# Kernel tuning notes

Hardware: AMD Instinct MI355X
Metric: run time of the kernel (lower is better)

Reference implementation:

```python
import jax, jax.numpy as jnp
import numpy as np

B, S, H = 8, 4096, 2048
E, F, K = 32, 128, 2
UTIL_BONUS = 0.1
CAP_PENALTY = 0.1


def setup_inputs() -> dict:
    key = jax.random.key(0)
    ks = jax.random.split(key, 4)
    hidden = jax.random.normal(ks[0], (B, S, H), dtype=jnp.float32)
    router_w = 0.02 * jax.random.normal(ks[1], (E, H), dtype=jnp.float32)
    router_b = jnp.zeros((E,), dtype=jnp.float32)
    w1 = 0.02 * jax.random.normal(ks[2], (E, F, H), dtype=jnp.float32)
    b1 = jnp.zeros((E, F), dtype=jnp.float32)
    w2 = 0.02 * jax.random.normal(ks[3], (E, H, F), dtype=jnp.float32)
    b2 = jnp.zeros((E, H), dtype=jnp.float32)
    activation_counts = jnp.zeros((E,), dtype=jnp.float32)
    expert_drift = jnp.zeros((E,), dtype=jnp.float32)
    return {"hidden": hidden, "router_w": router_w, "router_b": router_b,
            "w1": w1, "b1": b1, "w2": w2, "b2": b2,
            "activation_counts": activation_counts, "expert_drift": expert_drift}


def reference(hidden, router_w, router_b, w1, b1, w2, b2, activation_counts, expert_drift):
    # --- router with usage bonus / capacity penalty (buffers are zero at init) ---
    pooled = hidden.mean(axis=1)                      # [B, H]
    base_logits = pooled @ router_w.T + router_b      # [B, E]
    total = activation_counts.sum()
    usage = activation_counts / jnp.maximum(total, 1e-8)
    bonus = jnp.where(total > 0.0, UTIL_BONUS * (1.0 - usage), jnp.zeros_like(usage))
    usage_norm = activation_counts / jnp.maximum(activation_counts.max(), 1e-8)
    drift_norm = expert_drift / jnp.maximum(expert_drift.max(), 1e-8)
    penalty = CAP_PENALTY * 0.5 * (usage_norm + drift_norm)
    logits = base_logits + bonus[None, :] - penalty[None, :]
    router_probs = jax.nn.softmax(logits, axis=-1)    # [B, E]

    topk_probs, topk_idx = jax.lax.top_k(router_probs, K)  # [B, K]
    topk_probs = topk_probs / jnp.maximum(topk_probs.sum(axis=-1, keepdims=True), 1e-8)

    # --- gather selected expert weights and apply to the full sequence ---
    W1 = w1[topk_idx]   # [B, K, F, H]
    B1 = b1[topk_idx]   # [B, K, F]
    W2 = w2[topk_idx]   # [B, K, H, F]
    B2 = b2[topk_idx]   # [B, K, H]

    h1 = jnp.einsum('bsh,bkfh->bksf', hidden, W1) + B1[:, :, None, :]
    h1 = jax.nn.gelu(h1, approximate=False)           # torch nn.GELU default = exact erf
    out = jnp.einsum('bksf,bkhf->bksh', h1, W2) + B2[:, :, None, :]
    delta = jnp.einsum('bk,bksh->bsh', topk_probs, out)  # weighted combine
    return delta, topk_idx, topk_probs, router_probs
```

## Files before the change

kernel.cpp:

```cpp
#include <hip/hip_runtime.h>
#include <hip/hip_bf16.h>

#define BB 8
#define SS 4096
#define HH 2048
#define EE 32
#define FF 128

constexpr size_t DELTA_N = (size_t)BB * SS * HH;
constexpr size_t WELEM = (size_t)EE * FF * HH;
constexpr size_t WBYTES = WELEM * 2;

typedef short bf16x8 __attribute__((ext_vector_type(8)));
typedef float f32x4 __attribute__((ext_vector_type(4)));
typedef unsigned short u16;
typedef __attribute__((address_space(3))) unsigned char as3u8;
typedef __attribute__((address_space(1))) const unsigned char as1u8;

__device__ __forceinline__ u16 f2bfu(float x) {
  unsigned int u = __float_as_uint(x);
  u = (u + 0x7FFFu + ((u >> 16) & 1u)) >> 16;
  return (u16)u;
}

__device__ __forceinline__ unsigned int pk2(float a, float b) {
  union { __hip_bfloat162 h; unsigned int u; } c;
  c.h = __float22bfloat162_rn(make_float2(a, b));
  return c.u;
}

__device__ __forceinline__ bf16x8 pack8(float4 a, float4 b) {
  union { bf16x8 v; unsigned int u[4]; } r;
  r.u[0] = pk2(a.x, a.y);
  r.u[1] = pk2(a.z, a.w);
  r.u[2] = pk2(b.x, b.y);
  r.u[3] = pk2(b.z, b.w);
  return r.v;
}

__device__ __forceinline__ uint4 cvt4(float4 a, float4 b) {
  return make_uint4(pk2(a.x, a.y), pk2(a.z, a.w), pk2(b.x, b.y), pk2(b.z, b.w));
}

__device__ __forceinline__ void glds16(const void* g, void* l) {
  __builtin_amdgcn_global_load_lds((as1u8*)g, (as3u8*)l, 16, 0, 0);
}

__global__ void k_zero(float* __restrict__ ws) {
  if (threadIdx.x < 288) ws[threadIdx.x] = 0.0f;
}

__global__ void k_pool_logits(const float* __restrict__ hidden,
                              const float* __restrict__ rw,
                              float* __restrict__ logits) {
  const int b  = blockIdx.x >> 6;
  const int hc = (blockIdx.x >> 3) & 7;
  const int sq = blockIdx.x & 7;
  const int t  = threadIdx.x;
  const int tx = t & 63;
  const int qq = t >> 6;
  const int h0 = hc * 256;

  const float* p = hidden + ((size_t)b * SS + sq * 512 + qq * 128) * HH + h0 + tx * 4;
  float4 s = make_float4(0.f, 0.f, 0.f, 0.f);
  for (int i = 0; i < 128; ++i) {
    float4 v = *(const float4*)(p + (size_t)i * HH);
    s.x += v.x; s.y += v.y; s.z += v.z; s.w += v.w;
  }
  __shared__ float ps[4][256];
  __shared__ float pl[256];
  *(float4*)&ps[qq][tx * 4] = s;
  __syncthreads();
  pl[t] = ps[0][t] + ps[1][t] + ps[2][t] + ps[3][t];
  __syncthreads();

  const int e = t >> 3, part = t & 7;
  const float* wrp = rw + (size_t)e * HH + h0 + part * 32;
  float v = 0.f;
#pragma unroll
  for (int m = 0; m < 32; ++m) v += pl[part * 32 + m] * wrp[m];
  v += __shfl_xor(v, 1, 8);
  v += __shfl_xor(v, 2, 8);
  v += __shfl_xor(v, 4, 8);
  if (part == 0) atomicAdd(&logits[b * EE + e], v * (1.0f / (float)SS));
}

__global__ void k_topk(const float* __restrict__ logits, const float* __restrict__ rb,
                       const float* __restrict__ counts, const float* __restrict__ drift,
                       int* __restrict__ sel, float* __restrict__ pscale,
                       float* __restrict__ out) {
  int t = threadIdx.x;
  int b = t >> 5, e = t & 31;
  float total = 0.0f, cmax = 0.0f, dmax = 0.0f;
  for (int i = 0; i < EE; ++i) {
    float c = counts[i]; total += c; cmax = fmaxf(cmax, c);
    float d = drift[i];  dmax = fmaxf(dmax, d);
  }
  float cnt = counts[e], dr = drift[e];
  float usage = cnt / fmaxf(total, 1e-8f);
  float bonus = (total > 0.0f) ? 0.1f * (1.0f - usage) : 0.0f;
  float un = cnt / fmaxf(cmax, 1e-8f);
  float dn = dr / fmaxf(dmax, 1e-8f);
  float l = logits[t] + rb[e] + bonus - 0.05f * (un + dn);

  float m = l;
  for (int w = 16; w; w >>= 1) m = fmaxf(m, __shfl_xor(m, w, 32));
  float p = expf(l - m);
  float ssum = p;
  for (int w = 16; w; w >>= 1) ssum += __shfl_xor(ssum, w, 32);
  float prob = p / ssum;
  out[DELTA_N + 32 + t] = prob;

  float v1 = prob; int i1 = e;
  for (int w = 16; w; w >>= 1) {
    float ov = __shfl_xor(v1, w, 32); int oi = __shfl_xor(i1, w, 32);
    if (ov > v1 || (ov == v1 && oi < i1)) { v1 = ov; i1 = oi; }
  }
  float v2 = (e == i1) ? -1.0f : prob; int i2 = e;
  for (int w = 16; w; w >>= 1) {
    float ov = __shfl_xor(v2, w, 32); int oi = __shfl_xor(i2, w, 32);
    if (ov > v2 || (ov == v2 && oi < i2)) { v2 = ov; i2 = oi; }
  }
  if (e == 0) {
    float denom = fmaxf(v1 + v2, 1e-8f);
    float tp0 = v1 / denom, tp1 = v2 / denom;
    sel[b * 2 + 0] = i1;
    sel[b * 2 + 1] = i2;
    pscale[b * 2 + 0] = tp0;
    pscale[b * 2 + 1] = tp1;
    out[DELTA_N + 0 + b * 2 + 0] = (float)i1;
    out[DELTA_N + 0 + b * 2 + 1] = (float)i2;
    out[DELTA_N + 16 + b * 2 + 0] = tp0;
    out[DELTA_N + 16 + b * 2 + 1] = tp1;
  }
}

__global__ void k_pack(const float* __restrict__ w1, const float* __restrict__ w2,
                       u16* __restrict__ w1p, u16* __restrict__ w2p) {
  unsigned c = blockIdx.x * 256 + threadIdx.x;
  const float* src;
  u16* dst;
  if (c < 1048576u) {
    unsigned e = c >> 15, ci = c & 32767u;
    unsigned it = ci >> 10;
    unsigned cb = (ci & 1023u) * 16u;
    unsigned col = cb >> 7;
    unsigned kb = (cb & 127u) ^ ((col & 7u) << 4);
    unsigned k = it * 64u + (kb >> 1);
    src = w1 + ((size_t)(e * 128u + col) * HH + k);
    dst = w1p + (size_t)c * 8;
  } else {
    unsigned c2 = c - 1048576u;
    unsigned e = c2 >> 15, ci = c2 & 32767u;
    unsigned h = ci >> 4;
    unsigned cb = (ci & 15u) * 16u;
    unsigned kb = cb ^ ((h & 7u) << 4);
    unsigned f = kb >> 1;
    src = w2 + ((size_t)(e * 2048u + h) * FF + f);
    dst = w2p + (size_t)c2 * 8;
  }
  float4 a = *(const float4*)src;
  float4 b = *(const float4*)(src + 4);
  *(bf16x8*)dst = pack8(a, b);
}

#define SB_OFF 32768
#define T_OFF 65536

__global__ __launch_bounds__(512, 2) void k_ffn2(
    const float* __restrict__ hidden, const float* __restrict__ bs1,
    const float* __restrict__ bs2, const u16* __restrict__ w1p,
    const u16* __restrict__ w2p, const int* __restrict__ sel,
    const float* __restrict__ pscale, float* __restrict__ out) {
  __shared__ __align__(16) char smem[131072];

  const int t    = threadIdx.x;
  const int lane = t & 63;
  const int wv   = t >> 6;
  const int wr   = wv >> 2;
  const int wc   = wv & 3;
  const int l15  = lane & 15;
  const int lk   = lane >> 4;

  const int bid = blockIdx.x;
  const int b   = bid & 7;
  const int s0  = (bid >> 3) * 128;

  const int e0 = sel[2 * b], e1 = sel[2 * b + 1];
  const float p0 = pscale[2 * b], p1 = pscale[2 * b + 1];

  const int RB  = wr * 64;
  const int CBc = wc * 64;
  const int CB2 = wc * 32;

  const char* w1pb = (const char*)w1p;
  const char* w2pb = (const char*)w2p;

  const int arow = t >> 2;
  const int akq2 = (t & 3) * 32;
  const float* hA = hidden + ((size_t)b * SS + s0 + arow) * HH + (t & 3) * 16;
  const unsigned swA = (arow & 7) << 4;

  const size_t esel = (size_t)(wv < 4 ? e0 : e1);
  const char* w1src = w1pb + esel * 524288 + (size_t)(wv & 3) * 4096 + (size_t)lane * 16;
  char* sbW = &smem[SB_OFF + wv * 4096];

  f32x4 zero = {0.f, 0.f, 0.f, 0.f};
  f32x4 acc1[4][4];
#pragma unroll
  for (int i = 0; i < 4; ++i)
#pragma unroll
    for (int j = 0; j < 4; ++j) acc1[i][j] = zero;

  {
    float4 P[4];
#pragma unroll
    for (int q = 0; q < 4; ++q) P[q] = *(const float4*)(hA + q * 4);
#pragma unroll
    for (int r = 0; r < 4; ++r) glds16(w1src + r * 1024, sbW + r * 1024);
    char* da = &smem[arow * 128];
    *(uint4*)(da + (akq2 ^ swA)) = cvt4(P[0], P[1]);
    *(uint4*)(da + ((akq2 + 16) ^ swA)) = cvt4(P[2], P[3]);
  }
  __syncthreads();

  for (int j = 0; j < 32; ++j) {
    const int cb = j & 1, nb = cb ^ 1;
    float4 P[4];
    if (j < 31) {
      const float* hp = hA + (j + 1) * 64;
#pragma unroll
      for (int q = 0; q < 4; ++q) P[q] = *(const float4*)(hp + q * 4);
      const char* s = w1src + (size_t)(j + 1) * 16384;
      char* d = sbW + nb * 32768;
#pragma unroll
      for (int r = 0; r < 4; ++r) glds16(s + r * 1024, d + r * 1024);
    }
    const char* sa = &smem[cb * 16384];
    const char* sb = &smem[SB_OFF + cb * 32768];
#pragma unroll
    for (int kk = 0; kk < 2; ++kk) {
      bf16x8 af[4], bfv[4];
#pragma unroll
      for (int rt = 0; rt < 4; ++rt) {
        int row = RB + rt * 16 + l15;
        af[rt] = *(const bf16x8*)(sa + row * 128 + ((kk * 64 + lk * 16) ^ ((row & 7) << 4)));
      }
#pragma unroll
      for (int ct = 0; ct < 4; ++ct) {
        int col = CBc + ct * 16 + l15;
        bfv[ct] = *(const bf16x8*)(sb + col * 128 + ((kk * 64 + lk * 16) ^ ((col & 7) << 4)));
      }
#pragma unroll
      for (int rt = 0; rt < 4; ++rt)
#pragma unroll
        for (int ct = 0; ct < 4; ++ct)
          acc1[rt][ct] = __builtin_amdgcn_mfma_f32_16x16x32_bf16(af[rt], bfv[ct], acc1[rt][ct], 0, 0, 0);
    }
    if (j < 31) {
      char* da = &smem[nb * 16384 + arow * 128];
      *(uint4*)(da + (akq2 ^ swA)) = cvt4(P[0], P[1]);
      *(uint4*)(da + ((akq2 + 16) ^ swA)) = cvt4(P[2], P[3]);
    }
    __syncthreads();
  }

#pragma unroll
  for (int ct = 0; ct < 4; ++ct) {
    int c = CBc + ct * 16 + l15;
    int ec = (c < 128) ? e0 : e1;
    float pc = (c < 128) ? p0 : p1;
    float bias = bs1[ec * FF + (c & 127)];
#pragma unroll
    for (int rt = 0; rt < 4; ++rt)
#pragma unroll
      for (int r = 0; r < 4; ++r) {
        int row = RB + rt * 16 + lk * 4 + r;
        float x = acc1[rt][ct][r] + bias;
        float g = 0.5f * x * (1.0f + erff(x * 0.70710678118654752f));
        *(u16*)&smem[row * 512 + ((c * 2) ^ ((row & 7) << 4))] = f2bfu(pc * g);
      }
  }
  {
    const char* s = w2pb + (size_t)e0 * 524288 + (size_t)wv * 4096 + (size_t)lane * 16;
    char* d = &smem[T_OFF + wv * 4096];
#pragma unroll
    for (int r = 0; r < 4; ++r) glds16(s + r * 1024, d + r * 1024);
  }
  __syncthreads();

  bf16x8 pa[4][8];
#pragma unroll
  for (int rt = 0; rt < 4; ++rt) {
    int row = RB + rt * 16 + l15;
    unsigned sw = (row & 7) << 4;
#pragma unroll
    for (int ks = 0; ks < 8; ++ks)
      pa[rt][ks] = *(const bf16x8*)&smem[row * 512 + ((ks * 64 + lk * 16) ^ sw)];
  }

  float* obase = out + ((size_t)b * SS + s0) * HH;
  const char* gsrc_w = w2pb + (size_t)wv * 4096 + (size_t)lane * 16;

#pragma unroll 1
  for (int n0 = 0; n0 < 16; ++n0) {
    f32x4 acc2[4][2];
#pragma unroll
    for (int i = 0; i < 4; ++i) { acc2[i][0] = zero; acc2[i][1] = zero; }

    {
      const char* s = gsrc_w + (size_t)e1 * 524288 + (size_t)n0 * 32768;
      char* d = &smem[T_OFF + 32768 + wv * 4096];
#pragma unroll
      for (int r = 0; r < 4; ++r) glds16(s + r * 1024, d + r * 1024);
    }
    {
      const char* tb = &smem[T_OFF];
#pragma unroll
      for (int ks = 0; ks < 4; ++ks) {
        bf16x8 bfv[2];
#pragma unroll
        for (int ct = 0; ct < 2; ++ct) {
          int col = CB2 + ct * 16 + l15;
          bfv[ct] = *(const bf16x8*)(tb + col * 256 + ((ks * 64 + lk * 16) ^ ((col & 7) << 4)));
        }
#pragma unroll
        for (int rt = 0; rt < 4; ++rt)
#pragma unroll
          for (int ct = 0; ct < 2; ++ct)
            acc2[rt][ct] = __builtin_amdgcn_mfma_f32_16x16x32_bf16(pa[rt][ks], bfv[ct], acc2[rt][ct], 0, 0, 0);
      }
    }
    __syncthreads();

    if (n0 < 15) {
      const char* s = gsrc_w + (size_t)e0 * 524288 + (size_t)(n0 + 1) * 32768;
      char* d = &smem[T_OFF + wv * 4096];
#pragma unroll
      for (int r = 0; r < 4; ++r) glds16(s + r * 1024, d + r * 1024);
    }
    {
      const char* tb = &smem[T_OFF + 32768];
#pragma unroll
      for (int ks = 0; ks < 4; ++ks) {
        bf16x8 bfv[2];
#pragma unroll
        for (int ct = 0; ct < 2; ++ct) {
          int col = CB2 + ct * 16 + l15;
          bfv[ct] = *(const bf16x8*)(tb + col * 256 + ((ks * 64 + lk * 16) ^ ((col & 7) << 4)));
        }
#pragma unroll
        for (int rt = 0; rt < 4; ++rt)
#pragma unroll
          for (int ct = 0; ct < 2; ++ct)
            acc2[rt][ct] = __builtin_amdgcn_mfma_f32_16x16x32_bf16(pa[rt][4 + ks], bfv[ct], acc2[rt][ct], 0, 0, 0);
      }
    }
#pragma unroll
    for (int ct = 0; ct < 2; ++ct) {
      int h = n0 * 128 + CB2 + ct * 16 + l15;
      float bias = p0 * bs2[(size_t)e0 * HH + h] + p1 * bs2[(size_t)e1 * HH + h];
#pragma unroll
      for (int rt = 0; rt < 4; ++rt)
#pragma unroll
        for (int r = 0; r < 4; ++r) {
          int row = RB + rt * 16 + lk * 4 + r;
          obase[(size_t)row * HH + h] = acc2[rt][ct][r] + bias;
        }
    }
    __syncthreads();
  }
}

__global__ __launch_bounds__(512, 2) void k_ffn_fb(
    const float* __restrict__ hidden, const float* __restrict__ w1,
    const float* __restrict__ b1, const float* __restrict__ w2,
    const float* __restrict__ b2, const int* __restrict__ sel,
    const float* __restrict__ pscale, float* __restrict__ out) {
  __shared__ unsigned char sA[2][64 * 128];
  __shared__ unsigned char sG[64 * 512];

  const int t    = threadIdx.x;
  const int lane = t & 63;
  const int wv   = t >> 6;
  const int wr   = wv >> 2;
  const int wc   = wv & 3;
  const int l15  = lane & 15;
  const int lk   = lane >> 4;

  const int bid = blockIdx.x;
  const int b   = bid & 7;
  const int s0  = (bid >> 3) * 64;

  const int e0 = sel[2 * b], e1 = sel[2 * b + 1];
  const float p0 = pscale[2 * b], p1 = pscale[2 * b + 1];

  const float* hbase = hidden + ((size_t)b * SS + s0) * HH;
  const int srow = t >> 4;
  const int skq  = t & 15;

  float4 R[2];
  const float* wp[4];
#pragma unroll
  for (int ct = 0; ct < 4; ++ct) {
    int cbase = wc * 64 + ct * 16;
    int ec = (cbase < 128) ? e0 : e1;
    int f  = (cbase & 127) + l15;
    wp[ct] = w1 + ((size_t)ec * FF + f) * HH + lk * 8;
  }

  f32x4 zero = {0.f, 0.f, 0.f, 0.f};
  f32x4 acc1[2][4];
#pragma unroll
  for (int i = 0; i < 2; ++i)
#pragma unroll
    for (int j = 0; j < 4; ++j) acc1[i][j] = zero;

#pragma unroll
  for (int p = 0; p < 2; ++p)
    R[p] = *(const float4*)(hbase + (size_t)(srow + 32 * p) * HH + skq * 4);
#pragma unroll
  for (int p = 0; p < 2; ++p) {
    int row = srow + 32 * p;
    int addr = row * 128 + ((skq * 8) ^ ((row & 7) << 4));
    *(uint2*)(&sA[0][addr]) = make_uint2(pk2(R[p].x, R[p].y), pk2(R[p].z, R[p].w));
  }
  __syncthreads();

  for (int it = 0; it < 32; ++it) {
    const int buf = it & 1;
    if (it < 31) {
      const int k0 = (it + 1) * 64;
#pragma unroll
      for (int p = 0; p < 2; ++p)
        R[p] = *(const float4*)(hbase + (size_t)(srow + 32 * p) * HH + k0 + skq * 4);
    }
#pragma unroll
    for (int kk = 0; kk < 2; ++kk) {
      bf16x8 a[2];
#pragma unroll
      for (int rt = 0; rt < 2; ++rt) {
        int row = wr * 32 + rt * 16 + l15;
        a[rt] = *(const bf16x8*)(&sA[buf][row * 128 + ((kk * 64 + lk * 16) ^ ((row & 7) << 4))]);
      }
#pragma unroll
      for (int ct = 0; ct < 4; ++ct) {
        const float* q = wp[ct] + it * 64 + kk * 32;
        bf16x8 bfr = pack8(*(const float4*)q, *(const float4*)(q + 4));
#pragma unroll
        for (int rt = 0; rt < 2; ++rt)
          acc1[rt][ct] = __builtin_amdgcn_mfma_f32_16x16x32_bf16(a[rt], bfr, acc1[rt][ct], 0, 0, 0);
      }
    }
    if (it < 31) {
#pragma unroll
      for (int p = 0; p < 2; ++p) {
        int row = srow + 32 * p;
        int addr = row * 128 + ((skq * 8) ^ ((row & 7) << 4));
        *(uint2*)(&sA[buf ^ 1][addr]) = make_uint2(pk2(R[p].x, R[p].y), pk2(R[p].z, R[p].w));
      }
    }
    __syncthreads();
  }

#pragma unroll
  for (int ct = 0; ct < 4; ++ct) {
    int c = wc * 64 + ct * 16 + l15;
    int ec = (c < 128) ? e0 : e1;
    float pc = (c < 128) ? p0 : p1;
    float bias = b1[ec * FF + (c & 127)];
#pragma unroll
    for (int rt = 0; rt < 2; ++rt)
#pragma unroll
      for (int r = 0; r < 4; ++r) {
        int row = wr * 32 + rt * 16 + lk * 4 + r;
        float x = acc1[rt][ct][r] + bias;
        float g = 0.5f * x * (1.0f + erff(x * 0.70710678118654752f));
        int addr = row * 512 + ((c * 2) ^ ((row & 7) << 4));
        *(u16*)(&sG[addr]) = f2bfu(pc * g);
      }
  }
  __syncthreads();

  bf16x8 pa[2][8];
#pragma unroll
  for (int rt = 0; rt < 2; ++rt) {
    int row = wr * 32 + rt * 16 + l15;
#pragma unroll
    for (int ks = 0; ks < 8; ++ks)
      pa[rt][ks] = *(const bf16x8*)(&sG[row * 512 + ((ks * 64 + lk * 16) ^ ((row & 7) << 4))]);
  }

  float* obase = out + ((size_t)b * SS + s0) * HH;
  for (int ct = 0; ct < 32; ++ct) {
    const int h = wc * 512 + ct * 16 + l15;
    f32x4 acc[2];
    acc[0] = zero; acc[1] = zero;
    const float* q0 = w2 + ((size_t)e0 * HH + h) * FF + lk * 8;
    const float* q1 = w2 + ((size_t)e1 * HH + h) * FF + lk * 8;
#pragma unroll
    for (int ks = 0; ks < 8; ++ks) {
      const float* q = (ks < 4 ? q0 : q1) + (ks & 3) * 32;
      bf16x8 bfr = pack8(*(const float4*)q, *(const float4*)(q + 4));
#pragma unroll
      for (int rt = 0; rt < 2; ++rt)
        acc[rt] = __builtin_amdgcn_mfma_f32_16x16x32_bf16(pa[rt][ks], bfr, acc[rt], 0, 0, 0);
    }
    float bias = p0 * b2[(size_t)e0 * HH + h] + p1 * b2[(size_t)e1 * HH + h];
#pragma unroll
    for (int rt = 0; rt < 2; ++rt)
#pragma unroll
      for (int r = 0; r < 4; ++r) {
        int row = wr * 32 + rt * 16 + lk * 4 + r;
        obase[(size_t)row * HH + h] = acc[rt][r] + bias;
      }
  }
}

extern "C" void kernel_launch(void* const* d_in, const int* in_sizes, int n_in,
                              void* d_out, int out_size, void* d_ws, size_t ws_size,
                              hipStream_t stream) {
  const float* hidden   = (const float*)d_in[0];
  const float* router_w = (const float*)d_in[1];
  const float* router_b = (const float*)d_in[2];
  const float* w1       = (const float*)d_in[3];
  const float* b1       = (const float*)d_in[4];
  const float* w2       = (const float*)d_in[5];
  const float* b2       = (const float*)d_in[6];
  const float* counts   = (const float*)d_in[7];
  const float* drift    = (const float*)d_in[8];
  float* out            = (float*)d_out;

  float* logits = (float*)d_ws;
  int*   sel    = (int*)(logits + 256);
  float* pscale = logits + 272;
  u16*   w1p    = (u16*)((char*)d_ws + 4096);
  u16*   w2p    = (u16*)((char*)d_ws + 4096 + WBYTES);

  const size_t need = 4096 + 2 * WBYTES + 64;
  const bool useP = ws_size >= need;

  k_zero<<<1, 288, 0, stream>>>(logits);
  if (useP) k_pack<<<8192, 256, 0, stream>>>(w1, w2, w1p, w2p);
  k_pool_logits<<<512, 256, 0, stream>>>(hidden, router_w, logits);
  k_topk<<<1, 256, 0, stream>>>(logits, router_b, counts, drift, sel, pscale, out);
  if (useP)
    k_ffn2<<<256, 512, 0, stream>>>(hidden, b1, b2, w1p, w2p, sel, pscale, out);
  else
    k_ffn_fb<<<512, 512, 0, stream>>>(hidden, w1, b1, w2, b2, sel, pscale, out);
}
```

Measured before the change: 271.9 us.

## Fuse pooling with bf16 hidden pre-conversion and tile FFN from packed bf16

```diff
diff --git a/kernel.cpp b/kernel.cpp
--- a/kernel.cpp
+++ b/kernel.cpp
@@ -10,6 +10,7 @@
 constexpr size_t DELTA_N = (size_t)BB * SS * HH;
 constexpr size_t WELEM = (size_t)EE * FF * HH;
 constexpr size_t WBYTES = WELEM * 2;
+constexpr size_t HB16_BYTES = (size_t)BB * SS * HH * 2;
 
 typedef short bf16x8 __attribute__((ext_vector_type(8)));
 typedef float f32x4 __attribute__((ext_vector_type(4)));
@@ -46,93 +47,9 @@
   __builtin_amdgcn_global_load_lds((as1u8*)g, (as3u8*)l, 16, 0, 0);
 }
 
-__global__ void k_zero(float* __restrict__ ws) {
-  if (threadIdx.x < 288) ws[threadIdx.x] = 0.0f;
-}
-
-__global__ void k_pool_logits(const float* __restrict__ hidden,
-                              const float* __restrict__ rw,
-                              float* __restrict__ logits) {
-  const int b  = blockIdx.x >> 6;
-  const int hc = (blockIdx.x >> 3) & 7;
-  const int sq = blockIdx.x & 7;
-  const int t  = threadIdx.x;
-  const int tx = t & 63;
-  const int qq = t >> 6;
-  const int h0 = hc * 256;
-
-  const float* p = hidden + ((size_t)b * SS + sq * 512 + qq * 128) * HH + h0 + tx * 4;
-  float4 s = make_float4(0.f, 0.f, 0.f, 0.f);
-  for (int i = 0; i < 128; ++i) {
-    float4 v = *(const float4*)(p + (size_t)i * HH);
-    s.x += v.x; s.y += v.y; s.z += v.z; s.w += v.w;
-  }
-  __shared__ float ps[4][256];
-  __shared__ float pl[256];
-  *(float4*)&ps[qq][tx * 4] = s;
-  __syncthreads();
-  pl[t] = ps[0][t] + ps[1][t] + ps[2][t] + ps[3][t];
-  __syncthreads();
-
-  const int e = t >> 3, part = t & 7;
-  const float* wrp = rw + (size_t)e * HH + h0 + part * 32;
-  float v = 0.f;
-#pragma unroll
-  for (int m = 0; m < 32; ++m) v += pl[part * 32 + m] * wrp[m];
-  v += __shfl_xor(v, 1, 8);
-  v += __shfl_xor(v, 2, 8);
-  v += __shfl_xor(v, 4, 8);
-  if (part == 0) atomicAdd(&logits[b * EE + e], v * (1.0f / (float)SS));
-}
-
-__global__ void k_topk(const float* __restrict__ logits, const float* __restrict__ rb,
-                       const float* __restrict__ counts, const float* __restrict__ drift,
-                       int* __restrict__ sel, float* __restrict__ pscale,
-                       float* __restrict__ out) {
-  int t = threadIdx.x;
-  int b = t >> 5, e = t & 31;
-  float total = 0.0f, cmax = 0.0f, dmax = 0.0f;
-  for (int i = 0; i < EE; ++i) {
-    float c = counts[i]; total += c; cmax = fmaxf(cmax, c);
-    float d = drift[i];  dmax = fmaxf(dmax, d);
-  }
-  float cnt = counts[e], dr = drift[e];
-  float usage = cnt / fmaxf(total, 1e-8f);
-  float bonus = (total > 0.0f) ? 0.1f * (1.0f - usage) : 0.0f;
-  float un = cnt / fmaxf(cmax, 1e-8f);
-  float dn = dr / fmaxf(dmax, 1e-8f);
-  float l = logits[t] + rb[e] + bonus - 0.05f * (un + dn);
-
-  float m = l;
-  for (int w = 16; w; w >>= 1) m = fmaxf(m, __shfl_xor(m, w, 32));
-  float p = expf(l - m);
-  float ssum = p;
-  for (int w = 16; w; w >>= 1) ssum += __shfl_xor(ssum, w, 32);
-  float prob = p / ssum;
-  out[DELTA_N + 32 + t] = prob;
-
-  float v1 = prob; int i1 = e;
-  for (int w = 16; w; w >>= 1) {
-    float ov = __shfl_xor(v1, w, 32); int oi = __shfl_xor(i1, w, 32);
-    if (ov > v1 || (ov == v1 && oi < i1)) { v1 = ov; i1 = oi; }
-  }
-  float v2 = (e == i1) ? -1.0f : prob; int i2 = e;
-  for (int w = 16; w; w >>= 1) {
-    float ov = __shfl_xor(v2, w, 32); int oi = __shfl_xor(i2, w, 32);
-    if (ov > v2 || (ov == v2 && oi < i2)) { v2 = ov; i2 = oi; }
-  }
-  if (e == 0) {
-    float denom = fmaxf(v1 + v2, 1e-8f);
-    float tp0 = v1 / denom, tp1 = v2 / denom;
-    sel[b * 2 + 0] = i1;
-    sel[b * 2 + 1] = i2;
-    pscale[b * 2 + 0] = tp0;
-    pscale[b * 2 + 1] = tp1;
-    out[DELTA_N + 0 + b * 2 + 0] = (float)i1;
-    out[DELTA_N + 0 + b * 2 + 1] = (float)i2;
-    out[DELTA_N + 16 + b * 2 + 0] = tp0;
-    out[DELTA_N + 16 + b * 2 + 1] = tp1;
-  }
+__global__ void k_zero(float* __restrict__ ws, int n) {
+  int i = blockIdx.x * 256 + threadIdx.x;
+  if (i < n) ws[i] = 0.0f;
 }
 
 __global__ void k_pack(const float* __restrict__ w1, const float* __restrict__ w2,
@@ -164,10 +81,275 @@
   *(bf16x8*)dst = pack8(a, b);
 }
 
-#define SB_OFF 32768
-#define T_OFF 65536
-
-__global__ __launch_bounds__(512, 2) void k_ffn2(
+__global__ __launch_bounds__(512) void k_pooltile(const float* __restrict__ hidden,
+                                                  u16* __restrict__ hb16,
+                                                  float* __restrict__ psum) {
+  const int b  = blockIdx.x >> 6;
+  const int st = blockIdx.x & 63;
+  const int t  = threadIdx.x;
+
+  const float* src = hidden + ((size_t)b * SS + st * 64) * HH + t * 4;
+  char* dbase = (char*)hb16 + (size_t)(b * 64 + st) * 262144 + (size_t)(t >> 4) * 8192;
+  const int kq = (t & 15) * 8;
+
+  float4 s = make_float4(0.f, 0.f, 0.f, 0.f);
+  for (int r = 0; r < 64; ++r) {
+    float4 v = *(const float4*)(src + (size_t)r * HH);
+    s.x += v.x; s.y += v.y; s.z += v.z; s.w += v.w;
+    *(uint2*)(dbase + r * 128 + (kq ^ ((r & 7) << 4))) =
+        make_uint2(pk2(v.x, v.y), pk2(v.z, v.w));
+  }
+  float* pp = psum + (size_t)b * HH + t * 4;
+  atomicAdd(pp + 0, s.x);
+  atomicAdd(pp + 1, s.y);
+  atomicAdd(pp + 2, s.z);
+  atomicAdd(pp + 3, s.w);
+}
+
+__global__ void k_logits(const float* __restrict__ psum, const float* __restrict__ rw,
+                         float* __restrict__ logits) {
+  int b = blockIdx.x >> 5;
+  int e = blockIdx.x & 31;
+  int tid = threadIdx.x;
+  float acc = 0.0f;
+  const float* ps = psum + (size_t)b * HH;
+  const float* wr = rw + (size_t)e * HH;
+  for (int h = tid; h < HH; h += 256) acc = fmaf(ps[h], wr[h], acc);
+  __shared__ float red[256];
+  red[tid] = acc;
+  __syncthreads();
+  for (int w = 128; w > 0; w >>= 1) {
+    if (tid < w) red[tid] += red[tid + w];
+    __syncthreads();
+  }
+  if (tid == 0) logits[blockIdx.x] = red[0] * (1.0f / (float)SS);
+}
+
+__global__ void k_topk(const float* __restrict__ logits, const float* __restrict__ rb,
+                       const float* __restrict__ counts, const float* __restrict__ drift,
+                       int* __restrict__ sel, float* __restrict__ pscale,
+                       float* __restrict__ out) {
+  int t = threadIdx.x;
+  int b = t >> 5, e = t & 31;
+  float total = 0.0f, cmax = 0.0f, dmax = 0.0f;
+  for (int i = 0; i < EE; ++i) {
+    float c = counts[i]; total += c; cmax = fmaxf(cmax, c);
+    float d = drift[i];  dmax = fmaxf(dmax, d);
+  }
+  float cnt = counts[e], dr = drift[e];
+  float usage = cnt / fmaxf(total, 1e-8f);
+  float bonus = (total > 0.0f) ? 0.1f * (1.0f - usage) : 0.0f;
+  float un = cnt / fmaxf(cmax, 1e-8f);
+  float dn = dr / fmaxf(dmax, 1e-8f);
+  float l = logits[t] + rb[e] + bonus - 0.05f * (un + dn);
+
+  float m = l;
+  for (int w = 16; w; w >>= 1) m = fmaxf(m, __shfl_xor(m, w, 32));
+  float p = expf(l - m);
+  float ssum = p;
+  for (int w = 16; w; w >>= 1) ssum += __shfl_xor(ssum, w, 32);
+  float prob = p / ssum;
+  out[DELTA_N + 32 + t] = prob;
+
+  float v1 = prob; int i1 = e;
+  for (int w = 16; w; w >>= 1) {
+    float ov = __shfl_xor(v1, w, 32); int oi = __shfl_xor(i1, w, 32);
+    if (ov > v1 || (ov == v1 && oi < i1)) { v1 = ov; i1 = oi; }
+  }
+  float v2 = (e == i1) ? -1.0f : prob; int i2 = e;
+  for (int w = 16; w; w >>= 1) {
+    float ov = __shfl_xor(v2, w, 32); int oi = __shfl_xor(i2, w, 32);
+    if (ov > v2 || (ov == v2 && oi < i2)) { v2 = ov; i2 = oi; }
+  }
+  if (e == 0) {
+    float denom = fmaxf(v1 + v2, 1e-8f);
+    float tp0 = v1 / denom, tp1 = v2 / denom;
+    sel[b * 2 + 0] = i1;
+    sel[b * 2 + 1] = i2;
+    pscale[b * 2 + 0] = tp0;
+    pscale[b * 2 + 1] = tp1;
+    out[DELTA_N + 0 + b * 2 + 0] = (float)i1;
+    out[DELTA_N + 0 + b * 2 + 1] = (float)i2;
+    out[DELTA_N + 16 + b * 2 + 0] = tp0;
+    out[DELTA_N + 16 + b * 2 + 1] = tp1;
+  }
+}
+
+__global__ __launch_bounds__(512, 4) void k_ffn2(
+    const u16* __restrict__ hb16, const float* __restrict__ bs1,
+    const float* __restrict__ bs2, const u16* __restrict__ w1p,
+    const u16* __restrict__ w2p, const int* __restrict__ sel,
+    const float* __restrict__ pscale, float* __restrict__ out) {
+  __shared__ __align__(16) char smem[81920];
+
+  const int t    = threadIdx.x;
+  const int lane = t & 63;
+  const int wv   = t >> 6;
+  const int l15  = lane & 15;
+  const int lk   = lane >> 4;
+
+  const int bid = blockIdx.x;
+  const int b   = bid & 7;
+  const int st  = bid >> 3;
+
+  const int e0 = sel[2 * b], e1 = sel[2 * b + 1];
+  const float p0 = pscale[2 * b], p1 = pscale[2 * b + 1];
+
+  const int wr = wv >> 2, wc = wv & 3;
+  const int RB = wr * 32, CB = wc * 64;
+
+  const char* hsrc = (const char*)hb16 + (size_t)(b * 64 + st) * 262144 + (size_t)t * 16;
+  const size_t eB1 = (size_t)((wv < 4) ? e0 : e1) * 524288;
+  const char* bsrc = (const char*)w1p + eB1 + (size_t)(wv & 3) * 4096 + (size_t)lane * 16;
+
+  f32x4 zero = {0.f, 0.f, 0.f, 0.f};
+  f32x4 acc1[2][4];
+#pragma unroll
+  for (int i = 0; i < 2; ++i)
+#pragma unroll
+    for (int j = 0; j < 4; ++j) acc1[i][j] = zero;
+
+  glds16(hsrc, &smem[(size_t)t * 16]);
+#pragma unroll
+  for (int r = 0; r < 4; ++r)
+    glds16(bsrc + r * 1024, &smem[16384 + wv * 4096 + r * 1024 + lane * 16]);
+  __syncthreads();
+
+  for (int j = 0; j < 32; ++j) {
+    const int cb = j & 1, nb = cb ^ 1;
+    if (j < 31) {
+      glds16(hsrc + (size_t)(j + 1) * 8192, &smem[nb * 8192 + (size_t)t * 16]);
+      const char* s = bsrc + (size_t)(j + 1) * 16384;
+      char* d = &smem[16384 + nb * 32768 + wv * 4096 + lane * 16];
+#pragma unroll
+      for (int r = 0; r < 4; ++r) glds16(s + r * 1024, d + r * 1024);
+    }
+    const char* sa = &smem[cb * 8192];
+    const char* sb = &smem[16384 + cb * 32768];
+#pragma unroll
+    for (int kk = 0; kk < 2; ++kk) {
+      bf16x8 af[2], bv[4];
+#pragma unroll
+      for (int rt = 0; rt < 2; ++rt) {
+        int row = RB + rt * 16 + l15;
+        af[rt] = *(const bf16x8*)(sa + row * 128 + ((kk * 64 + lk * 16) ^ ((row & 7) << 4)));
+      }
+#pragma unroll
+      for (int ct = 0; ct < 4; ++ct) {
+        int col = CB + ct * 16 + l15;
+        bv[ct] = *(const bf16x8*)(sb + col * 128 + ((kk * 64 + lk * 16) ^ ((col & 7) << 4)));
+      }
+#pragma unroll
+      for (int rt = 0; rt < 2; ++rt)
+#pragma unroll
+        for (int ct = 0; ct < 4; ++ct)
+          acc1[rt][ct] = __builtin_amdgcn_mfma_f32_16x16x32_bf16(af[rt], bv[ct], acc1[rt][ct], 0, 0, 0);
+    }
+    __syncthreads();
+  }
+
+#pragma unroll
+  for (int ct = 0; ct < 4; ++ct) {
+    int c = CB + ct * 16 + l15;
+    int ec = (c < 128) ? e0 : e1;
+    float pc = (c < 128) ? p0 : p1;
+    float bias = bs1[ec * FF + (c & 127)];
+#pragma unroll
+    for (int rt = 0; rt < 2; ++rt)
+#pragma unroll
+      for (int r = 0; r < 4; ++r) {
+        int row = RB + rt * 16 + lk * 4 + r;
+        float x = acc1[rt][ct][r] + bias;
+        float g = 0.5f * x * (1.0f + erff(x * 0.70710678118654752f));
+        *(u16*)&smem[row * 512 + ((c * 2) ^ ((row & 7) << 4))] = f2bfu(pc * g);
+      }
+  }
+  const size_t eB2 = (size_t)((wv < 4) ? e0 : e1) * 524288;
+  const char* tsrc = (const char*)w2p + eB2 + (size_t)(wv & 3) * 2048 + (size_t)lane * 16;
+  {
+    char* d = &smem[32768 + (wv >> 2) * 8192 + (wv & 3) * 2048 + lane * 16];
+#pragma unroll
+    for (int i = 0; i < 2; ++i) glds16(tsrc + i * 1024, d + i * 1024);
+  }
+  __syncthreads();
+
+  const int wr2 = wv & 3, wc2 = wv >> 2;
+  bf16x8 pa[8];
+  {
+    int row = wr2 * 16 + l15;
+    unsigned sw = (row & 7) << 4;
+#pragma unroll
+    for (int ks = 0; ks < 8; ++ks)
+      pa[ks] = *(const bf16x8*)&smem[row * 512 + ((ks * 64 + lk * 16) ^ sw)];
+  }
+
+  float* obase = out + ((size_t)b * SS + st * 64) * HH;
+  const int hin = wc2 * 16 + l15;
+
+#pragma unroll 1
+  for (int n0 = 0; n0 < 64; ++n0) {
+    const int cb = n0 & 1, nb = cb ^ 1;
+    if (n0 < 63) {
+      const char* s = tsrc + (size_t)(n0 + 1) * 8192;
+      char* d = &smem[32768 + nb * 16384 + (wv >> 2) * 8192 + (wv & 3) * 2048 + lane * 16];
+#pragma unroll
+      for (int i = 0; i < 2; ++i) glds16(s + i * 1024, d + i * 1024);
+    }
+    f32x4 acc2 = zero;
+    const char* tb = &smem[32768 + cb * 16384];
+#pragma unroll
+    for (int ks = 0; ks < 8; ++ks) {
+      bf16x8 bv = *(const bf16x8*)(tb + (ks >> 2) * 8192 + hin * 256 +
+                                   (((ks & 3) * 64 + lk * 16) ^ ((hin & 7) << 4)));
+      acc2 = __builtin_amdgcn_mfma_f32_16x16x32_bf16(pa[ks], bv, acc2, 0, 0, 0);
+    }
+    const int h = n0 * 32 + hin;
+    float bias = p0 * bs2[(size_t)e0 * HH + h] + p1 * bs2[(size_t)e1 * HH + h];
+#pragma unroll
+    for (int r = 0; r < 4; ++r) {
+      int row = wr2 * 16 + lk * 4 + r;
+      obase[(size_t)row * HH + h] = acc2[r] + bias;
+    }
+    __syncthreads();
+  }
+}
+
+__global__ void k_pool_logits(const float* __restrict__ hidden,
+                              const float* __restrict__ rw,
+                              float* __restrict__ logits) {
+  const int b  = blockIdx.x >> 6;
+  const int hc = (blockIdx.x >> 3) & 7;
+  const int sq = blockIdx.x & 7;
+  const int t  = threadIdx.x;
+  const int tx = t & 63;
+  const int qq = t >> 6;
+  const int h0 = hc * 256;
+
+  const float* p = hidden + ((size_t)b * SS + sq * 512 + qq * 128) * HH + h0 + tx * 4;
+  float4 s = make_float4(0.f, 0.f, 0.f, 0.f);
+  for (int i = 0; i < 128; ++i) {
+    float4 v = *(const float4*)(p + (size_t)i * HH);
+    s.x += v.x; s.y += v.y; s.z += v.z; s.w += v.w;
+  }
+  __shared__ float ps[4][256];
+  __shared__ float pl[256];
+  *(float4*)&ps[qq][tx * 4] = s;
+  __syncthreads();
+  pl[t] = ps[0][t] + ps[1][t] + ps[2][t] + ps[3][t];
+  __syncthreads();
+
+  const int e = t >> 3, part = t & 7;
+  const float* wrp = rw + (size_t)e * HH + h0 + part * 32;
+  float v = 0.f;
+#pragma unroll
+  for (int m = 0; m < 32; ++m) v += pl[part * 32 + m] * wrp[m];
+  v += __shfl_xor(v, 1, 8);
+  v += __shfl_xor(v, 2, 8);
+  v += __shfl_xor(v, 4, 8);
+  if (part == 0) atomicAdd(&logits[b * EE + e], v * (1.0f / (float)SS));
+}
+
+__global__ __launch_bounds__(512, 2) void k_ffn_mid(
     const float* __restrict__ hidden, const float* __restrict__ bs1,
     const float* __restrict__ bs2, const u16* __restrict__ w1p,
     const u16* __restrict__ w2p, const int* __restrict__ sel,
@@ -203,7 +385,7 @@
 
   const size_t esel = (size_t)(wv < 4 ? e0 : e1);
   const char* w1src = w1pb + esel * 524288 + (size_t)(wv & 3) * 4096 + (size_t)lane * 16;
-  char* sbW = &smem[SB_OFF + wv * 4096];
+  char* sbW = &smem[32768 + wv * 4096];
 
   f32x4 zero = {0.f, 0.f, 0.f, 0.f};
   f32x4 acc1[4][4];
@@ -237,7 +419,7 @@
       for (int r = 0; r < 4; ++r) glds16(s + r * 1024, d + r * 1024);
     }
     const char* sa = &smem[cb * 16384];
-    const char* sb = &smem[SB_OFF + cb * 32768];
+    const char* sb = &smem[32768 + cb * 32768];
 #pragma unroll
     for (int kk = 0; kk < 2; ++kk) {
       bf16x8 af[4], bfv[4];
@@ -283,7 +465,7 @@
   }
   {
     const char* s = w2pb + (size_t)e0 * 524288 + (size_t)wv * 4096 + (size_t)lane * 16;
-    char* d = &smem[T_OFF + wv * 4096];
+    char* d = &smem[65536 + wv * 4096];
 #pragma unroll
     for (int r = 0; r < 4; ++r) glds16(s + r * 1024, d + r * 1024);
   }
@@ -307,15 +489,14 @@
     f32x4 acc2[4][2];
 #pragma unroll
     for (int i = 0; i < 4; ++i) { acc2[i][0] = zero; acc2[i][1] = zero; }
-
     {
       const char* s = gsrc_w + (size_t)e1 * 524288 + (size_t)n0 * 32768;
-      char* d = &smem[T_OFF + 32768 + wv * 4096];
+      char* d = &smem[65536 + 32768 + wv * 4096];
 #pragma unroll
       for (int r = 0; r < 4; ++r) glds16(s + r * 1024, d + r * 1024);
     }
     {
-      const char* tb = &smem[T_OFF];
+      const char* tb = &smem[65536];
 #pragma unroll
       for (int ks = 0; ks < 4; ++ks) {
         bf16x8 bfv[2];
@@ -332,15 +513,14 @@
       }
     }
     __syncthreads();
-
     if (n0 < 15) {
       const char* s = gsrc_w + (size_t)e0 * 524288 + (size_t)(n0 + 1) * 32768;
-      char* d = &smem[T_OFF + wv * 4096];
+      char* d = &smem[65536 + wv * 4096];
 #pragma unroll
       for (int r = 0; r < 4; ++r) glds16(s + r * 1024, d + r * 1024);
     }
     {
-      const char* tb = &smem[T_OFF + 32768];
+      const char* tb = &smem[65536 + 32768];
 #pragma unroll
       for (int ks = 0; ks < 4; ++ks) {
         bf16x8 bfv[2];
@@ -369,151 +549,6 @@
         }
     }
     __syncthreads();
-  }
-}
-
-__global__ __launch_bounds__(512, 2) void k_ffn_fb(
-    const float* __restrict__ hidden, const float* __restrict__ w1,
-    const float* __restrict__ b1, const float* __restrict__ w2,
-    const float* __restrict__ b2, const int* __restrict__ sel,
-    const float* __restrict__ pscale, float* __restrict__ out) {
-  __shared__ unsigned char sA[2][64 * 128];
-  __shared__ unsigned char sG[64 * 512];
-
-  const int t    = threadIdx.x;
-  const int lane = t & 63;
-  const int wv   = t >> 6;
-  const int wr   = wv >> 2;
-  const int wc   = wv & 3;
-  const int l15  = lane & 15;
-  const int lk   = lane >> 4;
-
-  const int bid = blockIdx.x;
-  const int b   = bid & 7;
-  const int s0  = (bid >> 3) * 64;
-
-  const int e0 = sel[2 * b], e1 = sel[2 * b + 1];
-  const float p0 = pscale[2 * b], p1 = pscale[2 * b + 1];
-
-  const float* hbase = hidden + ((size_t)b * SS + s0) * HH;
-  const int srow = t >> 4;
-  const int skq  = t & 15;
-
-  float4 R[2];
-  const float* wp[4];
-#pragma unroll
-  for (int ct = 0; ct < 4; ++ct) {
-    int cbase = wc * 64 + ct * 16;
-    int ec = (cbase < 128) ? e0 : e1;
-    int f  = (cbase & 127) + l15;
-    wp[ct] = w1 + ((size_t)ec * FF + f) * HH + lk * 8;
-  }
-
-  f32x4 zero = {0.f, 0.f, 0.f, 0.f};
-  f32x4 acc1[2][4];
-#pragma unroll
-  for (int i = 0; i < 2; ++i)
-#pragma unroll
-    for (int j = 0; j < 4; ++j) acc1[i][j] = zero;
-
-#pragma unroll
-  for (int p = 0; p < 2; ++p)
-    R[p] = *(const float4*)(hbase + (size_t)(srow + 32 * p) * HH + skq * 4);
-#pragma unroll
-  for (int p = 0; p < 2; ++p) {
-    int row = srow + 32 * p;
-    int addr = row * 128 + ((skq * 8) ^ ((row & 7) << 4));
-    *(uint2*)(&sA[0][addr]) = make_uint2(pk2(R[p].x, R[p].y), pk2(R[p].z, R[p].w));
-  }
-  __syncthreads();
-
-  for (int it = 0; it < 32; ++it) {
-    const int buf = it & 1;
-    if (it < 31) {
-      const int k0 = (it + 1) * 64;
-#pragma unroll
-      for (int p = 0; p < 2; ++p)
-        R[p] = *(const float4*)(hbase + (size_t)(srow + 32 * p) * HH + k0 + skq * 4);
-    }
-#pragma unroll
-    for (int kk = 0; kk < 2; ++kk) {
-      bf16x8 a[2];
-#pragma unroll
-      for (int rt = 0; rt < 2; ++rt) {
-        int row = wr * 32 + rt * 16 + l15;
-        a[rt] = *(const bf16x8*)(&sA[buf][row * 128 + ((kk * 64 + lk * 16) ^ ((row & 7) << 4))]);
-      }
-#pragma unroll
-      for (int ct = 0; ct < 4; ++ct) {
-        const float* q = wp[ct] + it * 64 + kk * 32;
-        bf16x8 bfr = pack8(*(const float4*)q, *(const float4*)(q + 4));
-#pragma unroll
-        for (int rt = 0; rt < 2; ++rt)
-          acc1[rt][ct] = __builtin_amdgcn_mfma_f32_16x16x32_bf16(a[rt], bfr, acc1[rt][ct], 0, 0, 0);
-      }
-    }
-    if (it < 31) {
-#pragma unroll
-      for (int p = 0; p < 2; ++p) {
-        int row = srow + 32 * p;
-        int addr = row * 128 + ((skq * 8) ^ ((row & 7) << 4));
-        *(uint2*)(&sA[buf ^ 1][addr]) = make_uint2(pk2(R[p].x, R[p].y), pk2(R[p].z, R[p].w));
-      }
-    }
-    __syncthreads();
-  }
-
-#pragma unroll
-  for (int ct = 0; ct < 4; ++ct) {
-    int c = wc * 64 + ct * 16 + l15;
-    int ec = (c < 128) ? e0 : e1;
-    float pc = (c < 128) ? p0 : p1;
-    float bias = b1[ec * FF + (c & 127)];
-#pragma unroll
-    for (int rt = 0; rt < 2; ++rt)
-#pragma unroll
-      for (int r = 0; r < 4; ++r) {
-        int row = wr * 32 + rt * 16 + lk * 4 + r;
-        float x = acc1[rt][ct][r] + bias;
-        float g = 0.5f * x * (1.0f + erff(x * 0.70710678118654752f));
-        int addr = row * 512 + ((c * 2) ^ ((row & 7) << 4));
-        *(u16*)(&sG[addr]) = f2bfu(pc * g);
-      }
-  }
-  __syncthreads();
-
-  bf16x8 pa[2][8];
-#pragma unroll
-  for (int rt = 0; rt < 2; ++rt) {
-    int row = wr * 32 + rt * 16 + l15;
-#pragma unroll
-    for (int ks = 0; ks < 8; ++ks)
-      pa[rt][ks] = *(const bf16x8*)(&sG[row * 512 + ((ks * 64 + lk * 16) ^ ((row & 7) << 4))]);
-  }
-
-  float* obase = out + ((size_t)b * SS + s0) * HH;
-  for (int ct = 0; ct < 32; ++ct) {
-    const int h = wc * 512 + ct * 16 + l15;
-    f32x4 acc[2];
-    acc[0] = zero; acc[1] = zero;
-    const float* q0 = w2 + ((size_t)e0 * HH + h) * FF + lk * 8;
-    const float* q1 = w2 + ((size_t)e1 * HH + h) * FF + lk * 8;
-#pragma unroll
-    for (int ks = 0; ks < 8; ++ks) {
-      const float* q = (ks < 4 ? q0 : q1) + (ks & 3) * 32;
-      bf16x8 bfr = pack8(*(const float4*)q, *(const float4*)(q + 4));
-#pragma unroll
-      for (int rt = 0; rt < 2; ++rt)
-        acc[rt] = __builtin_amdgcn_mfma_f32_16x16x32_bf16(pa[rt][ks], bfr, acc[rt], 0, 0, 0);
-    }
-    float bias = p0 * b2[(size_t)e0 * HH + h] + p1 * b2[(size_t)e1 * HH + h];
-#pragma unroll
-    for (int rt = 0; rt < 2; ++rt)
-#pragma unroll
-      for (int r = 0; r < 4; ++r) {
-        int row = wr * 32 + rt * 16 + lk * 4 + r;
-        obase[(size_t)row * HH + h] = acc[rt][r] + bias;
-      }
   }
 }
 
@@ -532,20 +567,30 @@
   float* out            = (float*)d_out;
 
   float* logits = (float*)d_ws;
-  int*   sel    = (int*)(logits + 256);
-  float* pscale = logits + 272;
-  u16*   w1p    = (u16*)((char*)d_ws + 4096);
-  u16*   w2p    = (u16*)((char*)d_ws + 4096 + WBYTES);
-
-  const size_t need = 4096 + 2 * WBYTES + 64;
-  const bool useP = ws_size >= need;
-
-  k_zero<<<1, 288, 0, stream>>>(logits);
-  if (useP) k_pack<<<8192, 256, 0, stream>>>(w1, w2, w1p, w2p);
-  k_pool_logits<<<512, 256, 0, stream>>>(hidden, router_w, logits);
-  k_topk<<<1, 256, 0, stream>>>(logits, router_b, counts, drift, sel, pscale, out);
-  if (useP)
-    k_ffn2<<<256, 512, 0, stream>>>(hidden, b1, b2, w1p, w2p, sel, pscale, out);
-  else
-    k_ffn_fb<<<512, 512, 0, stream>>>(hidden, w1, b1, w2, b2, sel, pscale, out);
-}
+  int*   sel    = (int*)((char*)d_ws + 1024);
+  float* pscale = (float*)((char*)d_ws + 1088);
+  float* psum   = (float*)((char*)d_ws + 4096);
+
+  const size_t need_big = 131072 + 2 * WBYTES + HB16_BYTES;
+  const size_t need_mid = 4096 + 2 * WBYTES + 64;
+
+  if (ws_size >= need_big) {
+    u16* w1p  = (u16*)((char*)d_ws + 131072);
+    u16* w2p  = (u16*)((char*)d_ws + 131072 + WBYTES);
+    u16* hb16 = (u16*)((char*)d_ws + 131072 + 2 * WBYTES);
+    k_zero<<<68, 256, 0, stream>>>(logits, 17408);
+    k_pack<<<8192, 256, 0, stream>>>(w1, w2, w1p, w2p);
+    k_pooltile<<<512, 512, 0, stream>>>(hidden, hb16, psum);
+    k_logits<<<256, 256, 0, stream>>>(psum, router_w, logits);
+    k_topk<<<1, 256, 0, stream>>>(logits, router_b, counts, drift, sel, pscale, out);
+    k_ffn2<<<512, 512, 0, stream>>>(hb16, b1, b2, w1p, w2p, sel, pscale, out);
+  } else if (ws_size >= need_mid) {
+    u16* w1p = (u16*)((char*)d_ws + 4096);
+    u16* w2p = (u16*)((char*)d_ws + 4096 + WBYTES);
+    k_zero<<<2, 256, 0, stream>>>(logits, 288);
+    k_pack<<<8192, 256, 0, stream>>>(w1, w2, w1p, w2p);
+    k_pool_logits<<<512, 256, 0, stream>>>(hidden, router_w, logits);
+    k_topk<<<1, 256, 0, stream>>>(logits, router_b, counts, drift, sel, pscale, out);
+    k_ffn_mid<<<256, 512, 0, stream>>>(hidden, b1, b2, w1p, w2p, sel, pscale, out);
+  }
+}
```

After: 304.7 us. 12.1% more time.
